# Kernel optimization log

Measured on AMD Instinct MI355X. Metric: run time of the kernel, lower is better.

## Reference

```python
import jax, jax.numpy as jnp
import numpy as np

# model dims
B, L, C, P, D, NB = 8, 512, 862, 96, 128, 2   # batch, seq_len, enc_in, pred_len, d_model, e_layers
I = 2 * D                                     # mLSTM inner (up-projection factor 2)
NH = 4                                        # mLSTM heads
DH = I // NH                                  # head dim
KDEC = 25                                     # series-decomp moving-average kernel
CK = 4                                        # causal conv kernel in mLSTM layer
EPS = 1e-5


def _ln(x, g):
    m = jnp.mean(x, -1, keepdims=True)
    v = jnp.var(x, -1, keepdims=True)
    return (x - m) * jax.lax.rsqrt(v + EPS) * g


def _mlstm_block(x, p):
    """Pre-LN residual mLSTM block (parallel stabilized formulation)."""
    (lng, Wup, bup, Wc, bc, Wq, Wk, Wv, Wi, bi, Wf, bf, mhg, skip, Wdn, bdn) = p
    Bn, S, _ = x.shape
    y = _ln(x, lng)
    up = y @ Wup + bup                       # [B,S,2I]
    x_in, z = jnp.split(up, 2, axis=-1)      # [B,S,I] each
    # causal depthwise conv (kernel CK) + SiLU
    xc = jax.lax.conv_general_dilated(
        x_in, Wc, window_strides=(1,), padding=((CK - 1, 0),),
        dimension_numbers=('NWC', 'WIO', 'NWC'), feature_group_count=I) + bc
    xc = jax.nn.silu(xc)
    q = xc @ Wq
    k = xc @ Wk
    v = x_in @ Wv
    g_in = jnp.concatenate([q, k, v], -1)    # [B,S,3I]
    ig = (g_in @ Wi + bi).transpose(0, 2, 1)  # [B,NH,S] input-gate preact
    fg = (g_in @ Wf + bf).transpose(0, 2, 1)  # [B,NH,S] forget-gate preact
    qh = q.reshape(Bn, S, NH, DH).transpose(0, 2, 1, 3)
    kh = k.reshape(Bn, S, NH, DH).transpose(0, 2, 1, 3) * (DH ** -0.5)
    vh = v.reshape(Bn, S, NH, DH).transpose(0, 2, 1, 3)
    logf = jax.nn.log_sigmoid(fg)            # [B,NH,S]
    cum = jnp.cumsum(logf, -1)               # inclusive cumsum
    # logD[t,s] = sum_{u=s+1..t} logf_u + i_s  (s<=t)
    logD = cum[..., :, None] - cum[..., None, :] + ig[..., None, :]
    mask = jnp.tril(jnp.ones((S, S), bool))
    logD = jnp.where(mask, logD, -jnp.inf)
    m = jnp.max(logD, -1, keepdims=True)     # row-wise stabilizer [B,NH,S,1]
    Dm = jnp.exp(logD - m)
    scores = jnp.einsum('bhtd,bhsd->bhts', qh, kh) * Dm
    norm = jnp.maximum(jnp.abs(jnp.sum(scores, -1, keepdims=True)), jnp.exp(-m))
    h = jnp.einsum('bhts,bhsd->bhtd', scores / norm, vh)  # [B,NH,S,DH]
    h = h.transpose(0, 2, 1, 3)              # [B,S,NH,DH]
    # multi-head layernorm (per-head, weight only)
    mu = jnp.mean(h, -1, keepdims=True)
    va = jnp.var(h, -1, keepdims=True)
    hn = ((h - mu) * jax.lax.rsqrt(va + EPS)).reshape(Bn, S, I) * mhg
    hs = (hn + skip * xc) * jax.nn.silu(z)
    return x + hs @ Wdn + bdn


def setup_inputs() -> dict:
    key = jax.random.key(0)
    ks = iter(jax.random.split(key, 32))
    f32 = jnp.float32
    def n(shape, s=0.02):
        return jax.random.normal(next(ks), shape, dtype=f32) * s
    inp = {
        'x_enc': jax.random.normal(next(ks), (B, L, C), f32),
        'x_mark_enc': jax.random.normal(next(ks), (B, L, 4), f32),
        'x_dec': jax.random.normal(next(ks), (B, P, C), f32),
        'x_mark_dec': jax.random.normal(next(ks), (B, P, 4), f32),
        # DLinear-style heads (init 1/seq_len as in the source)
        'Ws': jnp.full((P, L), 1.0 / L, dtype=f32), 'bs': jnp.zeros((P,), f32),
        'Wt': jnp.full((P, L), 1.0 / L, dtype=f32), 'bt': jnp.zeros((P,), f32),
        'Wp1': n((D, P)), 'bp1': jnp.zeros((D,), f32),
        'Wp2': n((P, D)), 'bp2': jnp.zeros((P,), f32),
        # stacked per-block mLSTM params
        'ln_g': jnp.ones((NB, D), f32),
        'Wup': n((NB, D, 2 * I)), 'bup': jnp.zeros((NB, 2 * I), f32),
        'Wconv': n((NB, CK, 1, I), 0.1), 'bconv': jnp.zeros((NB, I), f32),
        'Wq': n((NB, I, I)), 'Wk': n((NB, I, I)), 'Wv': n((NB, I, I)),
        'Wi': n((NB, 3 * I, NH)), 'bi': jnp.zeros((NB, NH), f32),
        'Wf': n((NB, 3 * I, NH)), 'bf': jnp.full((NB, NH), 3.0, dtype=f32),
        'mh_g': jnp.ones((NB, I), f32), 'skip': jnp.ones((NB, I), f32),
        'Wdn': n((NB, I, D)), 'bdn': jnp.zeros((NB, D), f32),
        'post_g': jnp.ones((D,), f32),
    }
    return inp


def reference(x_enc, x_mark_enc, x_dec, x_mark_dec, Ws, bs, Wt, bt, Wp1, bp1,
              Wp2, bp2, ln_g, Wup, bup, Wconv, bconv, Wq, Wk, Wv, Wi, bi, Wf,
              bf, mh_g, skip, Wdn, bdn, post_g):
    # series decomposition: edge-replicated moving average (kernel 25, stride 1)
    pad = (KDEC - 1) // 2
    front = jnp.repeat(x_enc[:, :1, :], pad, axis=1)
    end = jnp.repeat(x_enc[:, -1:, :], pad, axis=1)
    xp = jnp.concatenate([front, x_enc, end], axis=1)          # [B,L+24,C]
    cs = jnp.concatenate([jnp.zeros_like(xp[:, :1]), jnp.cumsum(xp, 1)], 1)
    mm = (cs[:, KDEC:, :] - cs[:, :-KDEC, :]) / KDEC           # [B,L,C]
    res = x_enc - mm
    si = res.transpose(0, 2, 1)                                # [B,C,L]
    ti = mm.transpose(0, 2, 1)
    x = (si @ Ws.T + bs) + (ti @ Wt.T + bt)                    # [B,C,P]
    x = x @ Wp1.T + bp1                                        # [B,C,D]
    for b in range(NB):
        x = _mlstm_block(x, (ln_g[b], Wup[b], bup[b], Wconv[b], bconv[b],
                             Wq[b], Wk[b], Wv[b], Wi[b], bi[b], Wf[b], bf[b],
                             mh_g[b], skip[b], Wdn[b], bdn[b]))
    x = _ln(x, post_g)
    x = x @ Wp2.T + bp2                                        # [B,C,P]
    return x.transpose(0, 2, 1)                                # [B,P,C]
```

## Files before the change

kernel.cpp:

```cpp
#include <hip/hip_runtime.h>
#include <math.h>

#define BB 8
#define LL 512
#define CC 862
#define PP 96
#define DD 128
#define II 256
#define NHH 4
#define DHH 64
#define SS 862
#define BC (BB*CC)
#define VTS 864
#define NITEMS2 896

typedef unsigned short u16;
using bf16x8 = __attribute__((ext_vector_type(8))) short;
using f32x4  = __attribute__((ext_vector_type(4))) float;

__device__ __forceinline__ u16 f2b(float x) {
  union { float f; unsigned u; } v; v.f = x;
  unsigned r = v.u + 0x7FFF + ((v.u >> 16) & 1);
  return (u16)(r >> 16);
}
__device__ __forceinline__ float b2f(u16 h) {
  union { unsigned u; float f; } v; v.u = ((unsigned)h) << 16;
  return v.f;
}

#define XCH(r, c) ((((c) ^ ((r) & 7)) << 3))

__global__ __launch_bounds__(256) void prep_kernel(
    const float* __restrict__ Wup, const float* __restrict__ Wq,
    const float* __restrict__ Wk, const float* __restrict__ Wv,
    const float* __restrict__ Wdn, const float* __restrict__ Ws,
    const float* __restrict__ Wt, const float* __restrict__ Wp1,
    const float* __restrict__ bs, const float* __restrict__ bt,
    const float* __restrict__ bp1, const float* __restrict__ Wi,
    const float* __restrict__ Wf,
    u16* __restrict__ WupT, u16* __restrict__ WqkT,
    u16* __restrict__ WvT, u16* __restrict__ WdnT,
    u16* __restrict__ BTh, float* __restrict__ hbias,
    float* __restrict__ Gc, float* __restrict__ Gv)
{
  int gb = blockIdx.x;
  int tid = threadIdx.x;
  if (gb < 640) {
    int bx = gb & 63, by = gb >> 6;
    const float* src; u16* dst; int R, Cn; float scl = 1.f;
    switch (by) {
      case 0: src = Wup;          dst = WupT;            R = 128; Cn = 512; break;
      case 1: src = Wup + 65536;  dst = WupT + 65536;    R = 128; Cn = 512; break;
      case 2: src = Wq;           dst = WqkT;            R = 256; Cn = 256; scl = 0.125f; break;
      case 3: src = Wk;           dst = WqkT + 65536;    R = 256; Cn = 256; break;
      case 4: src = Wq + 65536;   dst = WqkT + 131072;   R = 256; Cn = 256; scl = 0.125f; break;
      case 5: src = Wk + 65536;   dst = WqkT + 196608;   R = 256; Cn = 256; break;
      case 6: src = Wv;           dst = WvT;             R = 256; Cn = 256; break;
      case 7: src = Wv + 65536;   dst = WvT + 65536;     R = 256; Cn = 256; break;
      case 8: src = Wdn;          dst = WdnT;            R = 256; Cn = 128; break;
      default: src = Wdn + 32768; dst = WdnT + 32768;    R = 256; Cn = 128; break;
    }
    int tpr = Cn >> 5;
    int tx = bx % tpr, ty_ = bx / tpr;
    if (ty_ >= (R >> 5)) return;
    __shared__ float t[32][33];
    int r0 = ty_ * 32, c0 = tx * 32;
    int cr = tid >> 5, cc = tid & 31;
    #pragma unroll
    for (int rr = 0; rr < 4; ++rr)
      t[cr + rr * 8][cc] = src[(size_t)(r0 + cr + rr * 8) * Cn + c0 + cc];
    __syncthreads();
    #pragma unroll
    for (int rr = 0; rr < 4; ++rr)
      dst[(size_t)(c0 + cr + rr * 8) * R + r0 + cc] = f2b(t[cc][cr + rr * 8] * scl);
  } else if (gb < 1152) {
    int i2 = gb - 640;
    int d = i2 & 127, byy = i2 >> 7;
    int lp = byy * 256 + tid;
    const float* wp = Wp1 + d * 96;
    float acc = 0.f;
    if (lp < 512) {
      for (int p = 0; p < 96; ++p) acc += Ws[p * 512 + lp] * wp[p];
    } else {
      int l = lp - 512;
      for (int p = 0; p < 96; ++p) acc += (Wt[p * 512 + l] - Ws[p * 512 + l]) * wp[p];
    }
    BTh[(size_t)d * 1024 + lp] = f2b(acc);
  } else if (gb == 1152) {
    if (tid < 128) {
      float acc = bp1[tid];
      for (int p = 0; p < 96; ++p) acc += (bs[p] + bt[p]) * Wp1[tid * 96 + p];
      hbias[tid] = acc;
    }
  } else {
    int i2 = gb - 1153;
    int i = i2 & 255, blk = i2 >> 8;
    int j = tid;
    float wq = Wq[(size_t)blk * 65536 + i * 256 + j];
    float wk = Wk[(size_t)blk * 65536 + i * 256 + j];
    float wv = Wv[(size_t)blk * 65536 + i * 256 + j];
    const float* wi = Wi + blk * 3072;
    const float* wf = Wf + blk * 3072;
    float pc[8], pv[8];
    #pragma unroll
    for (int o = 0; o < 4; ++o) {
      pc[o]     = wq * wi[j * 4 + o] + wk * wi[(256 + j) * 4 + o];
      pc[4 + o] = wq * wf[j * 4 + o] + wk * wf[(256 + j) * 4 + o];
      pv[o]     = wv * wi[(512 + j) * 4 + o];
      pv[4 + o] = wv * wf[(512 + j) * 4 + o];
    }
    #pragma unroll
    for (int o = 0; o < 8; ++o)
      #pragma unroll
      for (int d = 1; d < 64; d <<= 1) {
        pc[o] += __shfl_xor(pc[o], d);
        pv[o] += __shfl_xor(pv[o], d);
      }
    __shared__ float red[4][16];
    int wv_ = j >> 6, lane = j & 63;
    if (lane == 0) {
      #pragma unroll
      for (int o = 0; o < 8; ++o) { red[wv_][o] = pc[o]; red[wv_][8 + o] = pv[o]; }
    }
    __syncthreads();
    if (j < 16) {
      float s4 = red[0][j] + red[1][j] + red[2][j] + red[3][j];
      if (j < 8) Gc[((size_t)blk * 256 + i) * 8 + j] = s4;
      else       Gv[((size_t)blk * 256 + i) * 8 + j - 8] = s4;
    }
  }
}

__global__ __launch_bounds__(256) void ta_kernel(
    const float* __restrict__ xe, u16* __restrict__ Ah)
{
  __shared__ float xel[16][545];
  __shared__ float mml[16][517];
  int tid = threadIdx.x;
  int b = blockIdx.x / 54, ct = blockIdx.x % 54;
  int c0 = ct * 16;
  for (int j = 0; j < 34; ++j) {
    int idx = tid + j * 256;
    if (idx < 8576) {
      int li = idx >> 4, cc = idx & 15;
      int l = li - 12; l = l < 0 ? 0 : (l > 511 ? 511 : l);
      int c = c0 + cc; if (c > 861) c = 861;
      xel[cc][li] = xe[((size_t)b * LL + l) * CC + c];
    }
  }
  __syncthreads();
  {
    int cl = tid & 15;
    int l0 = (tid >> 4) * 32;
    float win = 0.f;
    #pragma unroll 5
    for (int o = 0; o < 25; ++o) win += xel[cl][l0 + o];
    mml[cl][l0] = win * (1.f / 25.f);
    for (int i = 1; i < 32; ++i) {
      win += xel[cl][l0 + 24 + i] - xel[cl][l0 + i - 1];
      mml[cl][l0 + i] = win * (1.f / 25.f);
    }
  }
  __syncthreads();
  for (int j = 0; j < 32; ++j) {
    int idx = tid + j * 256;
    int cr = idx >> 9, l = idx & 511;
    int c = c0 + cr;
    if (c < CC) {
      size_t base = ((size_t)b * CC + c) * 1024;
      Ah[base + l] = f2b(xel[cr][12 + l]);
      Ah[base + 512 + l] = f2b(mml[cr][l]);
    }
  }
}

__device__ __forceinline__ void gemm_core(
    const u16* __restrict__ A, int lda, const u16* __restrict__ BT, int ldbt,
    int M, int K, int m0, int n0, int tid,
    u16 (*As0)[40], u16 (*As1)[40], u16 (*Bs0)[40], u16 (*Bs1)[40],
    f32x4 acc[2][2])
{
  int wv = tid >> 6, lane = tid & 63;
  int wr = wv >> 1, wc = wv & 1;
  int lrow = lane & 15, lk = lane >> 4;
  int arow = tid >> 2, aseg = tid & 3;
  for (int k0 = 0; k0 < K; k0 += 64) {
    int gm = m0 + arow; if (gm > M - 1) gm = M - 1;
    const u16* ap = &A[(size_t)gm * lda + k0 + aseg * 8];
    *(uint4*)&As0[arow][aseg * 8] = *(const uint4*)ap;
    *(uint4*)&As1[arow][aseg * 8] = *(const uint4*)(ap + 32);
    const u16* bp = &BT[(size_t)(n0 + arow) * ldbt + k0 + aseg * 8];
    *(uint4*)&Bs0[arow][aseg * 8] = *(const uint4*)bp;
    *(uint4*)&Bs1[arow][aseg * 8] = *(const uint4*)(bp + 32);
    __syncthreads();
    bf16x8 af[2], bfr[2];
    #pragma unroll
    for (int fm = 0; fm < 2; ++fm) af[fm] = *(const bf16x8*)&As0[wr * 32 + fm * 16 + lrow][lk * 8];
    #pragma unroll
    for (int fn = 0; fn < 2; ++fn) bfr[fn] = *(const bf16x8*)&Bs0[wc * 32 + fn * 16 + lrow][lk * 8];
    #pragma unroll
    for (int fm = 0; fm < 2; ++fm)
      #pragma unroll
      for (int fn = 0; fn < 2; ++fn)
        acc[fm][fn] = __builtin_amdgcn_mfma_f32_16x16x32_bf16(af[fm], bfr[fn], acc[fm][fn], 0, 0, 0);
    #pragma unroll
    for (int fm = 0; fm < 2; ++fm) af[fm] = *(const bf16x8*)&As1[wr * 32 + fm * 16 + lrow][lk * 8];
    #pragma unroll
    for (int fn = 0; fn < 2; ++fn) bfr[fn] = *(const bf16x8*)&Bs1[wc * 32 + fn * 16 + lrow][lk * 8];
    #pragma unroll
    for (int fm = 0; fm < 2; ++fm)
      #pragma unroll
      for (int fn = 0; fn < 2; ++fn)
        acc[fm][fn] = __builtin_amdgcn_mfma_f32_16x16x32_bf16(af[fm], bfr[fn], acc[fm][fn], 0, 0, 0);
    __syncthreads();
  }
}

template<int MODE>
__global__ __launch_bounds__(256) void gemm_bf16(
    const u16* __restrict__ A, int lda,
    const u16* __restrict__ BT, int ldbt,
    float* __restrict__ C, int ldc, const float* __restrict__ bias,
    int M, int N, int K)
{
  __shared__ u16 As0[64][40], As1[64][40];
  __shared__ u16 Bs0[64][40], Bs1[64][40];
  int tid = threadIdx.x;
  int m0 = blockIdx.y * 64, n0 = blockIdx.x * 64;
  f32x4 acc[2][2] = {};
  gemm_core(A, lda, BT, ldbt, M, K, m0, n0, tid, As0, As1, Bs0, Bs1, acc);
  int wv = tid >> 6, lane = tid & 63;
  int wr = wv >> 1, wc = wv & 1;
  int lrow = lane & 15, lk = lane >> 4;
  #pragma unroll
  for (int fm = 0; fm < 2; ++fm) {
    #pragma unroll
    for (int fn = 0; fn < 2; ++fn) {
      int col = n0 + wc * 32 + fn * 16 + lrow;
      #pragma unroll
      for (int r = 0; r < 4; ++r) {
        int row = m0 + wr * 32 + fm * 16 + lk * 4 + r;
        if (row < M) {
          float vv = acc[fm][fn][r];
          if (bias) vv += bias[col];
          float* cp = &C[(size_t)row * ldc + col];
          if (MODE == 1) vv += *cp;
          *cp = vv;
        }
      }
    }
  }
}

template<int MODE, int OUTF32, int FUSEC>
__global__ __launch_bounds__(256) void gemm_ln(
    const u16* __restrict__ A, int lda,
    const u16* __restrict__ BT, int ldbt,
    float* __restrict__ x, const float* __restrict__ bias,
    const float* __restrict__ g,
    float* __restrict__ y, u16* __restrict__ y_bf,
    int M, int K,
    const float* __restrict__ pacc, const float* __restrict__ pw,
    const float* __restrict__ cumf, const float* __restrict__ MMb,
    const float* __restrict__ up2, const float* __restrict__ xc2,
    const float* __restrict__ mhg, const float* __restrict__ skip)
{
  __shared__ u16 As0[32][40], As1[32][40];
  __shared__ u16 Bs0[128][40], Bs1[128][40];
  __shared__ float red_s[32][2], red_q[32][2];
  int tid = threadIdx.x;
  int m0 = blockIdx.x * 32;
  int wv = tid >> 6, lane = tid & 63;
  int wr = wv >> 1, wc = wv & 1;
  int lrow = lane & 15, lk = lane >> 4;
  f32x4 acc[4] = {};
  int arow = tid >> 3, aseg7 = tid & 7;
  int brow = tid >> 1, bhalf = tid & 1;
  for (int k0 = 0; k0 < K; k0 += 64) {
    int gm = m0 + arow; if (gm > M - 1) gm = M - 1;
    if (FUSEC == 0) {
      const u16* ap = &A[(size_t)gm * lda + k0];
      if (aseg7 < 4) *(uint4*)&As0[arow][aseg7 * 8] = *(const uint4*)(ap + aseg7 * 8);
      else           *(uint4*)&As1[arow][(aseg7 - 4) * 8] = *(const uint4*)(ap + 32 + (aseg7 - 4) * 8);
    } else {
      int bb = gm / SS, sx = gm - bb * SS;
      int hh = k0 >> 6;
      size_t bhS = ((size_t)bb * NHH + hh) * SS + sx;
      float wsum = pw[bhS] + pw[(size_t)BB * NHH * SS + bhS];
      float nfl = __expf(-(cumf[bhS] + MMb[bhS]));
      float rden = 1.f / fmaxf(fabsf(wsum), nfl);
      int colb = k0 + aseg7 * 8;
      const float* p0 = &pacc[(size_t)gm * II + colb];
      const float* p1 = p0 + (size_t)BC * II;
      float hv[8], sr = 0.f, sq2 = 0.f;
      #pragma unroll
      for (int j = 0; j < 8; ++j) {
        hv[j] = (p0[j] + p1[j]) * rden;
        sr += hv[j]; sq2 += hv[j] * hv[j];
      }
      sr += __shfl_xor(sr, 1); sq2 += __shfl_xor(sq2, 1);
      sr += __shfl_xor(sr, 2); sq2 += __shfl_xor(sq2, 2);
      sr += __shfl_xor(sr, 4); sq2 += __shfl_xor(sq2, 4);
      float mu = sr * (1.f / 64.f);
      float var = sq2 * (1.f / 64.f) - mu * mu;
      float rr2 = rsqrtf(var + 1e-5f);
      u16 o8[8];
      #pragma unroll
      for (int j = 0; j < 8; ++j) {
        int col = colb + j;
        float hn = (hv[j] - mu) * rr2 * mhg[col];
        float z = up2[(size_t)gm * 512 + 256 + col];
        float sil = z / (1.f + __expf(-z));
        o8[j] = f2b((hn + skip[col] * xc2[(size_t)gm * II + col]) * sil);
      }
      if (aseg7 < 4) *(uint4*)&As0[arow][aseg7 * 8] = *(const uint4*)o8;
      else           *(uint4*)&As1[arow][(aseg7 - 4) * 8] = *(const uint4*)o8;
    }
    const u16* bp = &BT[(size_t)brow * ldbt + k0];
    #pragma unroll
    for (int j = 0; j < 2; ++j) {
      int seg = bhalf * 2 + j;
      *(uint4*)&Bs0[brow][seg * 8] = *(const uint4*)(bp + seg * 8);
      *(uint4*)&Bs1[brow][seg * 8] = *(const uint4*)(bp + 32 + seg * 8);
    }
    __syncthreads();
    bf16x8 af, bfr[4];
    af = *(const bf16x8*)&As0[wr * 16 + lrow][lk * 8];
    #pragma unroll
    for (int fn = 0; fn < 4; ++fn) bfr[fn] = *(const bf16x8*)&Bs0[wc * 64 + fn * 16 + lrow][lk * 8];
    #pragma unroll
    for (int fn = 0; fn < 4; ++fn)
      acc[fn] = __builtin_amdgcn_mfma_f32_16x16x32_bf16(af, bfr[fn], acc[fn], 0, 0, 0);
    af = *(const bf16x8*)&As1[wr * 16 + lrow][lk * 8];
    #pragma unroll
    for (int fn = 0; fn < 4; ++fn) bfr[fn] = *(const bf16x8*)&Bs1[wc * 64 + fn * 16 + lrow][lk * 8];
    #pragma unroll
    for (int fn = 0; fn < 4; ++fn)
      acc[fn] = __builtin_amdgcn_mfma_f32_16x16x32_bf16(af, bfr[fn], acc[fn], 0, 0, 0);
    __syncthreads();
  }
  #pragma unroll
  for (int r = 0; r < 4; ++r) {
    int lrid = wr * 16 + lk * 4 + r;
    int grow = m0 + lrid;
    float sr = 0.f, sq = 0.f;
    #pragma unroll
    for (int fn = 0; fn < 4; ++fn) {
      int col = wc * 64 + fn * 16 + lrow;
      float vv = acc[fn][r] + bias[col];
      if (MODE == 1) vv += x[(size_t)grow * DD + col];
      acc[fn][r] = vv;
      if (grow < M) x[(size_t)grow * DD + col] = vv;
      sr += vv; sq += vv * vv;
    }
    sr += __shfl_xor(sr, 1); sq += __shfl_xor(sq, 1);
    sr += __shfl_xor(sr, 2); sq += __shfl_xor(sq, 2);
    sr += __shfl_xor(sr, 4); sq += __shfl_xor(sq, 4);
    sr += __shfl_xor(sr, 8); sq += __shfl_xor(sq, 8);
    if (lrow == 0) { red_s[lrid][wc] = sr; red_q[lrid][wc] = sq; }
  }
  __syncthreads();
  #pragma unroll
  for (int r = 0; r < 4; ++r) {
    int lrid = wr * 16 + lk * 4 + r;
    int grow = m0 + lrid;
    if (grow >= M) continue;
    float s = red_s[lrid][0] + red_s[lrid][1];
    float q = red_q[lrid][0] + red_q[lrid][1];
    float mean = s * (1.f / 128.f);
    float var = q * (1.f / 128.f) - mean * mean;
    float rr = rsqrtf(var + 1e-5f);
    #pragma unroll
    for (int fn = 0; fn < 4; ++fn) {
      int col = wc * 64 + fn * 16 + lrow;
      float out = (acc[fn][r] - mean) * rr * g[col];
      if (OUTF32) y[(size_t)grow * DD + col] = out;
      else        y_bf[(size_t)grow * DD + col] = f2b(out);
    }
  }
}

__device__ __forceinline__ float logsig(float x) {
  return fminf(x, 0.f) - log1pf(__expf(-fabsf(x)));
}

__global__ __launch_bounds__(256) void qkv_scan_kernel(
    const u16* __restrict__ xc_bf, const u16* __restrict__ xin_bf,
    const u16* __restrict__ WqkT, const u16* __restrict__ WvT,
    u16* __restrict__ qkh, u16* __restrict__ qkl,
    u16* __restrict__ vhT, u16* __restrict__ vlT,
    const float* __restrict__ fg, const float* __restrict__ ig,
    float* __restrict__ cumf, float* __restrict__ aa, float* __restrict__ MMb)
{
  __shared__ u16 As0[64][40], As1[64][40];
  __shared__ u16 Bs0[64][40], Bs1[64][40];
  int tid = threadIdx.x;
  int bx = blockIdx.x;
  if (bx >= 1296) {
    if (tid >= 64) return;
    int bh = bx - 1296;
    int lane = tid;
    const float* f = fg + (size_t)bh * SS;
    const float* gg = ig + (size_t)bh * SS;
    int s0 = lane * 14, s1 = s0 + 14; if (s1 > SS) s1 = SS;
    float loc = 0.f;
    for (int s = s0; s < s1; ++s) loc += logsig(f[s]);
    float v = loc;
    #pragma unroll
    for (int d = 1; d < 64; d <<= 1) { float o = __shfl_up(v, d); if (lane >= d) v += o; }
    float run = v - loc;
    float lmax = -1e30f;
    for (int s = s0; s < s1; ++s) {
      run += logsig(f[s]);
      cumf[(size_t)bh * SS + s] = run;
      float a = gg[s] - run;
      aa[(size_t)bh * SS + s] = a;
      lmax = fmaxf(lmax, a);
    }
    float mv = lmax;
    #pragma unroll
    for (int d = 1; d < 64; d <<= 1) { float o = __shfl_up(mv, d); if (lane >= d) mv = fmaxf(mv, o); }
    float em = __shfl_up(mv, 1);
    if (lane == 0) em = -1e30f;
    float runm = em;
    for (int s = s0; s < s1; ++s) {
      runm = fmaxf(runm, aa[(size_t)bh * SS + s]);
      MMb[(size_t)bh * SS + s] = runm;
    }
    return;
  }
  int m0 = (bx / 12) * 64;
  int nrole = bx % 12;
  bool is_qk = nrole < 8;
  int n0 = (is_qk ? nrole : nrole - 8) * 64;
  const u16* A  = is_qk ? xc_bf : xin_bf;
  const u16* BT = is_qk ? WqkT : WvT;
  f32x4 acc[2][2] = {};
  gemm_core(A, 256, BT, 256, BC, 256, m0, n0, tid, As0, As1, Bs0, Bs1, acc);
  int wv = tid >> 6, lane = tid & 63;
  int wr = wv >> 1, wc = wv & 1;
  int lrow = lane & 15, lk = lane >> 4;
  #pragma unroll
  for (int fm = 0; fm < 2; ++fm) {
    #pragma unroll
    for (int fn = 0; fn < 2; ++fn) {
      int col = n0 + wc * 32 + fn * 16 + lrow;
      int rbase = m0 + wr * 32 + fm * 16 + lk * 4;
      if (is_qk) {
        #pragma unroll
        for (int r = 0; r < 4; ++r) {
          int row = rbase + r;
          if (row < BC) {
            float vv = acc[fm][fn][r];
            u16 hi = f2b(vv);
            u16 lo = f2b(vv - b2f(hi));
            qkh[(size_t)row * 512 + col] = hi;
            qkl[(size_t)row * 512 + col] = lo;
          }
        }
      } else {
        u16 hi4[4], lo4[4];
        #pragma unroll
        for (int r = 0; r < 4; ++r) {
          float vv = acc[fm][fn][r];
          hi4[r] = f2b(vv);
          lo4[r] = f2b(vv - b2f(hi4[r]));
        }
        int bb0 = rbase / SS, s0_ = rbase - bb0 * SS;
        int bb3 = (rbase + 3) / SS;
        if (bb0 == bb3 && rbase + 3 < BC) {
          size_t o = ((size_t)bb0 * II + col) * VTS + s0_;
          *(unsigned*)&vhT[o]     = (unsigned)hi4[0] | ((unsigned)hi4[1] << 16);
          *(unsigned*)&vhT[o + 2] = (unsigned)hi4[2] | ((unsigned)hi4[3] << 16);
          *(unsigned*)&vlT[o]     = (unsigned)lo4[0] | ((unsigned)lo4[1] << 16);
          *(unsigned*)&vlT[o + 2] = (unsigned)lo4[2] | ((unsigned)lo4[3] << 16);
        } else {
          #pragma unroll
          for (int r = 0; r < 4; ++r) {
            int row = rbase + r;
            if (row < BC) {
              int bb = row / SS, s = row - bb * SS;
              size_t o = ((size_t)bb * II + col) * VTS + s;
              vhT[o] = hi4[r];
              vlT[o] = lo4[r];
            }
          }
        }
      }
    }
  }
}

__global__ __launch_bounds__(256) void conv_gates_kernel(
    const float* __restrict__ up, const float* __restrict__ Wc,
    const float* __restrict__ bc, const float* __restrict__ Gc,
    const float* __restrict__ Gv, const float* __restrict__ bi,
    const float* __restrict__ bfp,
    float* __restrict__ xc, u16* __restrict__ xc_bf, u16* __restrict__ xin_bf,
    float* __restrict__ ig, float* __restrict__ fg)
{
  __shared__ float red[4][8];
  int row = blockIdx.x;
  int i = threadIdx.x;
  int b = row / SS, s = row - b * SS;
  float acc = bc[i];
  float xin = 0.f;
  #pragma unroll
  for (int w2 = 0; w2 < 4; ++w2) {
    int sp = s - 3 + w2;
    if (sp >= 0) {
      float uv = up[((size_t)b * SS + sp) * 512 + i];
      acc += uv * Wc[w2 * 256 + i];
      if (w2 == 3) xin = uv;
    }
  }
  float sg = 1.f / (1.f + __expf(-acc));
  float val = acc * sg;
  xc[(size_t)row * II + i] = val;
  xc_bf[(size_t)row * II + i] = f2b(val);
  xin_bf[(size_t)row * II + i] = f2b(xin);
  float p[8];
  const float* gci = &Gc[i * 8];
  const float* gvi = &Gv[i * 8];
  #pragma unroll
  for (int o = 0; o < 8; ++o) p[o] = val * gci[o] + xin * gvi[o];
  #pragma unroll
  for (int o = 0; o < 8; ++o)
    #pragma unroll
    for (int d = 1; d < 64; d <<= 1) p[o] += __shfl_xor(p[o], d);
  int wv = i >> 6, lane = i & 63;
  if (lane == 0) {
    #pragma unroll
    for (int o = 0; o < 8; ++o) red[wv][o] = p[o];
  }
  __syncthreads();
  if (i < 8) {
    float sum = red[0][i] + red[1][i] + red[2][i] + red[3][i];
    if (i < 4) ig[((size_t)b * NHH + i) * SS + s] = sum + bi[i];
    else       fg[((size_t)b * NHH + i - 4) * SS + s] = sum + bfp[i - 4];
  }
}

__global__ __launch_bounds__(256) void attn_kernel(
    const u16* __restrict__ qkh, const u16* __restrict__ qkl,
    const u16* __restrict__ vhT, const u16* __restrict__ vlT,
    const float* __restrict__ aab, const float* __restrict__ MMb,
    float* __restrict__ pacc, float* __restrict__ pw)
{
  __shared__ u16 KWh[64][64], KWl[64][64];
  __shared__ u16 Vh[64][64], Vl[64][64];
  __shared__ float a_lds[64];
  int tid = threadIdx.x;
  int wv = tid >> 6, lane = tid & 63;
  int lr = lane & 15, lg = lane >> 4;
  int item = blockIdx.x;
  int pp = item >> 5;
  int tb = 13 - (pp >> 1);
  int part = pp & 1;
  int h = item & 3, b = (item >> 2) & 7;
  int t0 = tb * 64;
  int nt = tb + 1;
  int nt0 = (nt + 1) >> 1;
  int st_begin = part ? nt0 : 0;
  int st_end   = part ? nt : nt0;
  const float* aabh = aab + ((size_t)b * NHH + h) * SS;
  const float* Mbh  = MMb + ((size_t)b * NHH + h) * SS;

  int tq = t0 + wv * 16 + lr; if (tq > SS - 1) tq = SS - 1;
  const u16* qrow_h = qkh + ((size_t)b * SS + tq) * 512 + h * 64;
  const u16* qrow_l = qkl + ((size_t)b * SS + tq) * 512 + h * 64;
  bf16x8 qh0 = *(const bf16x8*)(qrow_h + lg * 8);
  bf16x8 qh1 = *(const bf16x8*)(qrow_h + 32 + lg * 8);
  bf16x8 ql0 = *(const bf16x8*)(qrow_l + lg * 8);
  bf16x8 ql1 = *(const bf16x8*)(qrow_l + 32 + lg * 8);

  float Mt[4];
  #pragma unroll
  for (int r = 0; r < 4; ++r) {
    int t = t0 + wv * 16 + lg * 4 + r; int tc = t < SS ? t : SS - 1;
    Mt[r] = Mbh[tc];
  }

  int row = tid >> 2, seg = tid & 3;
  const u16* vrow_h = vhT + ((size_t)(b * II + h * 64 + row)) * VTS + seg * 16;
  const u16* vrow_l = vlT + ((size_t)(b * II + h * 64 + row)) * VTS + seg * 16;

  f32x4 hacc[4] = {};
  float wsum[4] = {0.f, 0.f, 0.f, 0.f};

  uint4 rk0, rk1, rk2, rk3, rv0, rv1, rv2, rv3;
  float ra = -1e30f;
  if (st_begin < st_end) {
    int sg = st_begin * 64 + row;
    int sc = sg < SS ? sg : SS - 1;
    const u16* kp  = qkh + ((size_t)b * SS + sc) * 512 + 256 + h * 64 + seg * 16;
    const u16* klp = qkl + ((size_t)b * SS + sc) * 512 + 256 + h * 64 + seg * 16;
    rk0 = *(const uint4*)kp;  rk1 = *(const uint4*)(kp + 8);
    rk2 = *(const uint4*)klp; rk3 = *(const uint4*)(klp + 8);
    int sn = st_begin * 64;
    rv0 = *(const uint4*)(vrow_h + sn); rv1 = *(const uint4*)(vrow_h + sn + 8);
    rv2 = *(const uint4*)(vrow_l + sn); rv3 = *(const uint4*)(vrow_l + sn + 8);
    if (tid < 64) ra = (sn + tid < SS) ? aabh[sn + tid] : -1e30f;
  }

  for (int st = st_begin; st < st_end; ++st) {
    int s0 = st * 64;
    __syncthreads();
    *(uint4*)&KWh[row][XCH(row, 2 * seg)]     = rk0;
    *(uint4*)&KWh[row][XCH(row, 2 * seg + 1)] = rk1;
    *(uint4*)&KWl[row][XCH(row, 2 * seg)]     = rk2;
    *(uint4*)&KWl[row][XCH(row, 2 * seg + 1)] = rk3;
    *(uint4*)&Vh[row][XCH(row, 2 * seg)]     = rv0;
    *(uint4*)&Vh[row][XCH(row, 2 * seg + 1)] = rv1;
    *(uint4*)&Vl[row][XCH(row, 2 * seg)]     = rv2;
    *(uint4*)&Vl[row][XCH(row, 2 * seg + 1)] = rv3;
    if (tid < 64) a_lds[tid] = ra;
    if (st + 1 < st_end) {
      int sn = s0 + 64;
      int sg = sn + row;
      int sc = sg < SS ? sg : SS - 1;
      const u16* kp  = qkh + ((size_t)b * SS + sc) * 512 + 256 + h * 64 + seg * 16;
      const u16* klp = qkl + ((size_t)b * SS + sc) * 512 + 256 + h * 64 + seg * 16;
      rk0 = *(const uint4*)kp;  rk1 = *(const uint4*)(kp + 8);
      rk2 = *(const uint4*)klp; rk3 = *(const uint4*)(klp + 8);
      rv0 = *(const uint4*)(vrow_h + sn); rv1 = *(const uint4*)(vrow_h + sn + 8);
      rv2 = *(const uint4*)(vrow_l + sn); rv3 = *(const uint4*)(vrow_l + sn + 8);
      if (tid < 64) ra = (sn + tid < SS) ? aabh[sn + tid] : -1e30f;
    }
    __syncthreads();
    float am = a_lds[lane];
    #pragma unroll
    for (int dd = 1; dd < 64; dd <<= 1) am = fmaxf(am, __shfl_xor(am, dd));
    f32x4 p[4];
    #pragma unroll
    for (int sf = 0; sf < 4; ++sf) {
      int sr = sf * 16 + lr;
      bf16x8 kh0 = *(const bf16x8*)&KWh[sr][XCH(sr, lg)];
      bf16x8 kh1 = *(const bf16x8*)&KWh[sr][XCH(sr, lg + 4)];
      bf16x8 kl0 = *(const bf16x8*)&KWl[sr][XCH(sr, lg)];
      bf16x8 kl1 = *(const bf16x8*)&KWl[sr][XCH(sr, lg + 4)];
      f32x4 acc = {};
      acc = __builtin_amdgcn_mfma_f32_16x16x32_bf16(qh0, kl0, acc, 0, 0, 0);
      acc = __builtin_amdgcn_mfma_f32_16x16x32_bf16(qh1, kl1, acc, 0, 0, 0);
      acc = __builtin_amdgcn_mfma_f32_16x16x32_bf16(ql0, kh0, acc, 0, 0, 0);
      acc = __builtin_amdgcn_mfma_f32_16x16x32_bf16(ql1, kh1, acc, 0, 0, 0);
      acc = __builtin_amdgcn_mfma_f32_16x16x32_bf16(qh0, kh0, acc, 0, 0, 0);
      acc = __builtin_amdgcn_mfma_f32_16x16x32_bf16(qh1, kh1, acc, 0, 0, 0);
      p[sf] = acc;
    }
    __syncthreads();
    float ee[4], ft[4];
    #pragma unroll
    for (int sf = 0; sf < 4; ++sf) ee[sf] = __expf(a_lds[sf * 16 + lr] - am);
    #pragma unroll
    for (int r = 0; r < 4; ++r) ft[r] = __expf(fminf(am - Mt[r], 80.f));
    #pragma unroll
    for (int sf = 0; sf < 4; ++sf) {
      int s = s0 + sf * 16 + lr;
      int sc_ = sf * 2 + (lr >> 3), sb = lr & 7;
      #pragma unroll
      for (int r = 0; r < 4; ++r) {
        int tl_ = wv * 16 + lg * 4 + r;
        int t = t0 + tl_;
        float wval = (s <= t) ? p[sf][r] * ee[sf] * ft[r] : 0.f;
        wsum[r] += wval;
        u16 hi_ = f2b(wval);
        u16 lo_ = f2b(wval - b2f(hi_));
        KWh[tl_][XCH(tl_, sc_) + sb] = hi_;
        KWl[tl_][XCH(tl_, sc_) + sb] = lo_;
      }
    }
    __syncthreads();
    int tr = wv * 16 + lr;
    bf16x8 wh0 = *(const bf16x8*)&KWh[tr][XCH(tr, lg)];
    bf16x8 wh1 = *(const bf16x8*)&KWh[tr][XCH(tr, lg + 4)];
    bf16x8 wl0 = *(const bf16x8*)&KWl[tr][XCH(tr, lg)];
    bf16x8 wl1 = *(const bf16x8*)&KWl[tr][XCH(tr, lg + 4)];
    #pragma unroll
    for (int df = 0; df < 4; ++df) {
      int dr = df * 16 + lr;
      bf16x8 vh0 = *(const bf16x8*)&Vh[dr][XCH(dr, lg)];
      bf16x8 vh1 = *(const bf16x8*)&Vh[dr][XCH(dr, lg + 4)];
      bf16x8 vl0 = *(const bf16x8*)&Vl[dr][XCH(dr, lg)];
      bf16x8 vl1 = *(const bf16x8*)&Vl[dr][XCH(dr, lg + 4)];
      f32x4 a2 = hacc[df];
      a2 = __builtin_amdgcn_mfma_f32_16x16x32_bf16(wh0, vl0, a2, 0, 0, 0);
      a2 = __builtin_amdgcn_mfma_f32_16x16x32_bf16(wh1, vl1, a2, 0, 0, 0);
      a2 = __builtin_amdgcn_mfma_f32_16x16x32_bf16(wl0, vh0, a2, 0, 0, 0);
      a2 = __builtin_amdgcn_mfma_f32_16x16x32_bf16(wl1, vh1, a2, 0, 0, 0);
      a2 = __builtin_amdgcn_mfma_f32_16x16x32_bf16(wh0, vh0, a2, 0, 0, 0);
      a2 = __builtin_amdgcn_mfma_f32_16x16x32_bf16(wh1, vh1, a2, 0, 0, 0);
      hacc[df] = a2;
    }
  }
  #pragma unroll
  for (int r = 0; r < 4; ++r) {
    float sgn = wsum[r];
    sgn += __shfl_xor(sgn, 1); sgn += __shfl_xor(sgn, 2);
    sgn += __shfl_xor(sgn, 4); sgn += __shfl_xor(sgn, 8);
    wsum[r] = sgn;
  }
  float* pa = pacc + (size_t)part * BC * II;
  #pragma unroll
  for (int r = 0; r < 4; ++r) {
    int t = t0 + wv * 16 + lg * 4 + r;
    if (t < SS) {
      #pragma unroll
      for (int df = 0; df < 4; ++df)
        pa[((size_t)b * SS + t) * II + h * 64 + df * 16 + lr] = hacc[df][r];
      if (lr == 0)
        pw[(((size_t)part * BB + b) * NHH + h) * SS + t] = wsum[r];
    }
  }
}

__global__ __launch_bounds__(256) void final_kernel(
    const float* __restrict__ y, const float* __restrict__ Wp2,
    const float* __restrict__ bp2, float* __restrict__ out)
{
  __shared__ float yl[32 * 132];
  __shared__ float ol[96 * 32];
  int tid = threadIdx.x;
  int blk = blockIdx.x;
  int b = blk / 27, ct = blk % 27;
  int c0 = ct * 32;
  int nc = CC - c0; if (nc > 32) nc = 32;
  for (int j = 0; j < 16; ++j) {
    int idx = tid + j * 256;
    int cl = idx >> 7, d2 = idx & 127;
    yl[cl * 132 + d2] = (cl < nc) ? y[((size_t)b * CC + c0 + cl) * DD + d2] : 0.f;
  }
  __syncthreads();
  for (int j = 0; j < 12; ++j) {
    int o = tid + j * 256;
    int p = o >> 5, cl = o & 31;
    const float* wr = Wp2 + p * 128;
    float acc = bp2[p];
    #pragma unroll 8
    for (int d0 = 0; d0 < 128; d0 += 4) {
      float4 yv = *(const float4*)&yl[cl * 132 + d0];
      float4 wv = *(const float4*)&wr[d0];
      acc += yv.x * wv.x + yv.y * wv.y + yv.z * wv.z + yv.w * wv.w;
    }
    ol[p * 32 + cl] = acc;
  }
  __syncthreads();
  for (int j = 0; j < 12; ++j) {
    int o = tid + j * 256;
    int p = o >> 5, cl = o & 31;
    if (cl < nc) out[(size_t)b * PP * CC + (size_t)p * CC + c0 + cl] = ol[p * 32 + cl];
  }
}

extern "C" void kernel_launch(void* const* d_in, const int* in_sizes, int n_in,
                              void* d_out, int out_size, void* d_ws, size_t ws_size,
                              hipStream_t stream) {
  const float* xe   = (const float*)d_in[0];
  const float* Ws   = (const float*)d_in[4];
  const float* bs   = (const float*)d_in[5];
  const float* Wt_  = (const float*)d_in[6];
  const float* bt   = (const float*)d_in[7];
  const float* Wp1  = (const float*)d_in[8];
  const float* bp1  = (const float*)d_in[9];
  const float* Wp2  = (const float*)d_in[10];
  const float* bp2  = (const float*)d_in[11];
  const float* lng  = (const float*)d_in[12];
  const float* Wup  = (const float*)d_in[13];
  const float* bup  = (const float*)d_in[14];
  const float* Wcv  = (const float*)d_in[15];
  const float* bcv  = (const float*)d_in[16];
  const float* Wq   = (const float*)d_in[17];
  const float* Wk   = (const float*)d_in[18];
  const float* Wv   = (const float*)d_in[19];
  const float* Wi   = (const float*)d_in[20];
  const float* bi   = (const float*)d_in[21];
  const float* Wf   = (const float*)d_in[22];
  const float* bf_  = (const float*)d_in[23];
  const float* mhg  = (const float*)d_in[24];
  const float* skp  = (const float*)d_in[25];
  const float* Wdn  = (const float*)d_in[26];
  const float* bdn  = (const float*)d_in[27];
  const float* pg   = (const float*)d_in[28];
  float* out = (float*)d_out;

  float* w   = (float*)d_ws;
  float* x   = w;
  float* y   = x   + 882688;
  float* up  = y   + 882688;
  float* xc  = up  + 3530752;
  float* pacc = xc + 1765376;
  float* pw  = pacc + 3530752;
  float* ig  = pw  + 55168;
  float* fg  = ig  + 27584;
  float* cum = fg  + 27584;
  float* aab = cum + 27584;
  float* MMb = aab + 27584;
  float* hbias = MMb + 27584;
  float* Gc  = hbias + 128;
  float* Gv  = Gc + 4096;
  u16* ub    = (u16*)(Gv + 4096);
  u16* y_bf  = ub;            ub += 6896 * 128;
  u16* xc_bf = ub;            ub += 6896 * 256;
  u16* xin_bf = ub;           ub += 6896 * 256;
  u16* qkh   = ub;            ub += 6896 * 512;
  u16* qkl   = ub;            ub += 6896 * 512;
  u16* vhT   = ub;            ub += 8 * 256 * VTS;
  u16* vlT   = ub;            ub += 8 * 256 * VTS;
  u16* BTh   = ub;            ub += 131072;
  u16* WupT  = ub;            ub += 131072;
  u16* WqkT  = ub;            ub += 262144;
  u16* WvT   = ub;            ub += 131072;
  u16* WdnT  = ub;            ub += 65536;
  u16* Ah = (u16*)up;

  prep_kernel<<<1665, 256, 0, stream>>>(
      Wup, Wq, Wk, Wv, Wdn, Ws, Wt_, Wp1, bs, bt, bp1, Wi, Wf,
      WupT, WqkT, WvT, WdnT, BTh, hbias, Gc, Gv);

  ta_kernel<<<432, 256, 0, stream>>>(xe, Ah);
  gemm_ln<0, 0, 0><<<216, 256, 0, stream>>>(
      Ah, 1024, BTh, 1024, x, hbias, lng, nullptr, y_bf, BC, 1024,
      nullptr, nullptr, nullptr, nullptr, nullptr, nullptr, nullptr, nullptr);

  for (int blk = 0; blk < 2; ++blk) {
    gemm_bf16<0><<<dim3(8, 108), 256, 0, stream>>>(
        y_bf, 128, WupT + blk * 65536, 128, up, 512, bup + blk * 512, BC, 512, 128);
    conv_gates_kernel<<<6896, 256, 0, stream>>>(
        up, Wcv + blk * 1024, bcv + blk * 256, Gc + blk * 2048, Gv + blk * 2048,
        bi + blk * 4, bf_ + blk * 4, xc, xc_bf, xin_bf, ig, fg);
    qkv_scan_kernel<<<1328, 256, 0, stream>>>(
        xc_bf, xin_bf, WqkT + blk * 131072, WvT + blk * 65536,
        qkh, qkl, vhT, vlT, fg, ig, cum, aab, MMb);
    attn_kernel<<<NITEMS2, 256, 0, stream>>>(qkh, qkl, vhT, vlT, aab, MMb, pacc, pw);
    if (blk == 0)
      gemm_ln<1, 0, 1><<<216, 256, 0, stream>>>(
          nullptr, 0, WdnT, 256, x, bdn, lng + 128, nullptr, y_bf, BC, 256,
          pacc, pw, cum, MMb, up, xc, mhg, skp);
    else
      gemm_ln<1, 1, 1><<<216, 256, 0, stream>>>(
          nullptr, 0, WdnT + 32768, 256, x, bdn + 128, pg, y, nullptr, BC, 256,
          pacc, pw, cum, MMb, up, xc, mhg + 256, skp + 256);
  }

  final_kernel<<<216, 256, 0, stream>>>(y, Wp2, bp2, out);
}
```

Measured before the change: 255.3 us.

## Fuse decomposition into prep kernel and output projection into final LN GEMM

The series-decomposition kernel is merged into the weight-prep kernel as extra blocks, so both run in one launch. The final kernel is also removed: the last LayerNorm GEMM writes its normalized rows to shared memory and computes the Wp2 projection directly into the output. This removes two kernel launches and the fp32 round trip of the final activations through global memory. In exchange, larger shared-memory allocations apply to all blocks of the merged kernels, which may reduce occupancy.

```diff
diff --git a/kernel.cpp b/kernel.cpp
--- a/kernel.cpp
+++ b/kernel.cpp
@@ -30,22 +30,66 @@
 
 #define XCH(r, c) ((((c) ^ ((r) & 7)) << 3))
 
-__global__ __launch_bounds__(256) void prep_kernel(
+__global__ __launch_bounds__(256) void prep_ta_kernel(
     const float* __restrict__ Wup, const float* __restrict__ Wq,
     const float* __restrict__ Wk, const float* __restrict__ Wv,
     const float* __restrict__ Wdn, const float* __restrict__ Ws,
     const float* __restrict__ Wt, const float* __restrict__ Wp1,
     const float* __restrict__ bs, const float* __restrict__ bt,
     const float* __restrict__ bp1, const float* __restrict__ Wi,
-    const float* __restrict__ Wf,
+    const float* __restrict__ Wf, const float* __restrict__ xe,
     u16* __restrict__ WupT, u16* __restrict__ WqkT,
     u16* __restrict__ WvT, u16* __restrict__ WdnT,
     u16* __restrict__ BTh, float* __restrict__ hbias,
-    float* __restrict__ Gc, float* __restrict__ Gv)
+    float* __restrict__ Gc, float* __restrict__ Gv,
+    u16* __restrict__ Ah)
 {
+  __shared__ float smem[16 * 545 + 16 * 517];
   int gb = blockIdx.x;
   int tid = threadIdx.x;
+  if (gb >= 1665) {
+    float (*xel)[545] = (float(*)[545])smem;
+    float (*mml)[517] = (float(*)[517])(smem + 16 * 545);
+    int bx = gb - 1665;
+    int b = bx / 54, ct = bx % 54;
+    int c0 = ct * 16;
+    for (int j = 0; j < 34; ++j) {
+      int idx = tid + j * 256;
+      if (idx < 8576) {
+        int li = idx >> 4, cc = idx & 15;
+        int l = li - 12; l = l < 0 ? 0 : (l > 511 ? 511 : l);
+        int c = c0 + cc; if (c > 861) c = 861;
+        xel[cc][li] = xe[((size_t)b * LL + l) * CC + c];
+      }
+    }
+    __syncthreads();
+    {
+      int cl = tid & 15;
+      int l0 = (tid >> 4) * 32;
+      float win = 0.f;
+      #pragma unroll 5
+      for (int o = 0; o < 25; ++o) win += xel[cl][l0 + o];
+      mml[cl][l0] = win * (1.f / 25.f);
+      for (int i = 1; i < 32; ++i) {
+        win += xel[cl][l0 + 24 + i] - xel[cl][l0 + i - 1];
+        mml[cl][l0 + i] = win * (1.f / 25.f);
+      }
+    }
+    __syncthreads();
+    for (int j = 0; j < 32; ++j) {
+      int idx = tid + j * 256;
+      int cr = idx >> 9, l = idx & 511;
+      int c = c0 + cr;
+      if (c < CC) {
+        size_t base = ((size_t)b * CC + c) * 1024;
+        Ah[base + l] = f2b(xel[cr][12 + l]);
+        Ah[base + 512 + l] = f2b(mml[cr][l]);
+      }
+    }
+    return;
+  }
   if (gb < 640) {
+    float (*t)[33] = (float(*)[33])smem;
     int bx = gb & 63, by = gb >> 6;
     const float* src; u16* dst; int R, Cn; float scl = 1.f;
     switch (by) {
@@ -63,7 +107,6 @@
     int tpr = Cn >> 5;
     int tx = bx % tpr, ty_ = bx / tpr;
     if (ty_ >= (R >> 5)) return;
-    __shared__ float t[32][33];
     int r0 = ty_ * 32, c0 = tx * 32;
     int cr = tid >> 5, cc = tid & 31;
     #pragma unroll
@@ -93,6 +136,7 @@
       hbias[tid] = acc;
     }
   } else {
+    float (*red)[16] = (float(*)[16])smem;
     int i2 = gb - 1153;
     int i = i2 & 255, blk = i2 >> 8;
     int j = tid;
@@ -116,7 +160,6 @@
         pc[o] += __shfl_xor(pc[o], d);
         pv[o] += __shfl_xor(pv[o], d);
       }
-    __shared__ float red[4][16];
     int wv_ = j >> 6, lane = j & 63;
     if (lane == 0) {
       #pragma unroll
@@ -127,49 +170,6 @@
       float s4 = red[0][j] + red[1][j] + red[2][j] + red[3][j];
       if (j < 8) Gc[((size_t)blk * 256 + i) * 8 + j] = s4;
       else       Gv[((size_t)blk * 256 + i) * 8 + j - 8] = s4;
-    }
-  }
-}
-
-__global__ __launch_bounds__(256) void ta_kernel(
-    const float* __restrict__ xe, u16* __restrict__ Ah)
-{
-  __shared__ float xel[16][545];
-  __shared__ float mml[16][517];
-  int tid = threadIdx.x;
-  int b = blockIdx.x / 54, ct = blockIdx.x % 54;
-  int c0 = ct * 16;
-  for (int j = 0; j < 34; ++j) {
-    int idx = tid + j * 256;
-    if (idx < 8576) {
-      int li = idx >> 4, cc = idx & 15;
-      int l = li - 12; l = l < 0 ? 0 : (l > 511 ? 511 : l);
-      int c = c0 + cc; if (c > 861) c = 861;
-      xel[cc][li] = xe[((size_t)b * LL + l) * CC + c];
-    }
-  }
-  __syncthreads();
-  {
-    int cl = tid & 15;
-    int l0 = (tid >> 4) * 32;
-    float win = 0.f;
-    #pragma unroll 5
-    for (int o = 0; o < 25; ++o) win += xel[cl][l0 + o];
-    mml[cl][l0] = win * (1.f / 25.f);
-    for (int i = 1; i < 32; ++i) {
-      win += xel[cl][l0 + 24 + i] - xel[cl][l0 + i - 1];
-      mml[cl][l0 + i] = win * (1.f / 25.f);
-    }
-  }
-  __syncthreads();
-  for (int j = 0; j < 32; ++j) {
-    int idx = tid + j * 256;
-    int cr = idx >> 9, l = idx & 511;
-    int c = c0 + cr;
-    if (c < CC) {
-      size_t base = ((size_t)b * CC + c) * 1024;
-      Ah[base + l] = f2b(xel[cr][12 + l]);
-      Ah[base + 512 + l] = f2b(mml[cr][l]);
     }
   }
 }
@@ -252,7 +252,7 @@
   }
 }
 
-template<int MODE, int OUTF32, int FUSEC>
+template<int MODE, int OUTF32, int FUSEC, int FINAL>
 __global__ __launch_bounds__(256) void gemm_ln(
     const u16* __restrict__ A, int lda,
     const u16* __restrict__ BT, int ldbt,
@@ -263,11 +263,14 @@
     const float* __restrict__ pacc, const float* __restrict__ pw,
     const float* __restrict__ cumf, const float* __restrict__ MMb,
     const float* __restrict__ up2, const float* __restrict__ xc2,
-    const float* __restrict__ mhg, const float* __restrict__ skip)
+    const float* __restrict__ mhg, const float* __restrict__ skip,
+    const float* __restrict__ Wp2, const float* __restrict__ bp2,
+    float* __restrict__ out)
 {
   __shared__ u16 As0[32][40], As1[32][40];
   __shared__ u16 Bs0[128][40], Bs1[128][40];
   __shared__ float red_s[32][2], red_q[32][2];
+  __shared__ float yl[32][132];
   int tid = threadIdx.x;
   int m0 = blockIdx.x * 32;
   int wv = tid >> 6, lane = tid & 63;
@@ -364,7 +367,7 @@
   for (int r = 0; r < 4; ++r) {
     int lrid = wr * 16 + lk * 4 + r;
     int grow = m0 + lrid;
-    if (grow >= M) continue;
+    if (FINAL == 0 && grow >= M) continue;
     float s = red_s[lrid][0] + red_s[lrid][1];
     float q = red_q[lrid][0] + red_q[lrid][1];
     float mean = s * (1.f / 128.f);
@@ -373,9 +376,33 @@
     #pragma unroll
     for (int fn = 0; fn < 4; ++fn) {
       int col = wc * 64 + fn * 16 + lrow;
-      float out = (acc[fn][r] - mean) * rr * g[col];
-      if (OUTF32) y[(size_t)grow * DD + col] = out;
-      else        y_bf[(size_t)grow * DD + col] = f2b(out);
+      float outv = (acc[fn][r] - mean) * rr * g[col];
+      if (FINAL) {
+        yl[lrid][col] = outv;
+      } else if (OUTF32) {
+        y[(size_t)grow * DD + col] = outv;
+      } else {
+        y_bf[(size_t)grow * DD + col] = f2b(outv);
+      }
+    }
+  }
+  if (FINAL) {
+    __syncthreads();
+    for (int j = 0; j < 12; ++j) {
+      int o = tid + j * 256;
+      int p = o >> 5, cl = o & 31;
+      int grow = m0 + cl;
+      if (grow >= M) continue;
+      const float* wr2 = Wp2 + p * 128;
+      float accf = bp2[p];
+      #pragma unroll 8
+      for (int d0 = 0; d0 < 128; d0 += 4) {
+        float4 yv = *(const float4*)&yl[cl][d0];
+        float4 wv2 = *(const float4*)&wr2[d0];
+        accf += yv.x * wv2.x + yv.y * wv2.y + yv.z * wv2.z + yv.w * wv2.w;
+      }
+      int b = grow / SS, c = grow - b * SS;
+      out[(size_t)b * PP * CC + (size_t)p * CC + c] = accf;
     }
   }
 }
@@ -714,44 +741,6 @@
   }
 }
 
-__global__ __launch_bounds__(256) void final_kernel(
-    const float* __restrict__ y, const float* __restrict__ Wp2,
-    const float* __restrict__ bp2, float* __restrict__ out)
-{
-  __shared__ float yl[32 * 132];
-  __shared__ float ol[96 * 32];
-  int tid = threadIdx.x;
-  int blk = blockIdx.x;
-  int b = blk / 27, ct = blk % 27;
-  int c0 = ct * 32;
-  int nc = CC - c0; if (nc > 32) nc = 32;
-  for (int j = 0; j < 16; ++j) {
-    int idx = tid + j * 256;
-    int cl = idx >> 7, d2 = idx & 127;
-    yl[cl * 132 + d2] = (cl < nc) ? y[((size_t)b * CC + c0 + cl) * DD + d2] : 0.f;
-  }
-  __syncthreads();
-  for (int j = 0; j < 12; ++j) {
-    int o = tid + j * 256;
-    int p = o >> 5, cl = o & 31;
-    const float* wr = Wp2 + p * 128;
-    float acc = bp2[p];
-    #pragma unroll 8
-    for (int d0 = 0; d0 < 128; d0 += 4) {
-      float4 yv = *(const float4*)&yl[cl * 132 + d0];
-      float4 wv = *(const float4*)&wr[d0];
-      acc += yv.x * wv.x + yv.y * wv.y + yv.z * wv.z + yv.w * wv.w;
-    }
-    ol[p * 32 + cl] = acc;
-  }
-  __syncthreads();
-  for (int j = 0; j < 12; ++j) {
-    int o = tid + j * 256;
-    int p = o >> 5, cl = o & 31;
-    if (cl < nc) out[(size_t)b * PP * CC + (size_t)p * CC + c0 + cl] = ol[p * 32 + cl];
-  }
-}
-
 extern "C" void kernel_launch(void* const* d_in, const int* in_sizes, int n_in,
                               void* d_out, int out_size, void* d_ws, size_t ws_size,
                               hipStream_t stream) {
@@ -813,14 +802,14 @@
   u16* WdnT  = ub;            ub += 65536;
   u16* Ah = (u16*)up;
 
-  prep_kernel<<<1665, 256, 0, stream>>>(
-      Wup, Wq, Wk, Wv, Wdn, Ws, Wt_, Wp1, bs, bt, bp1, Wi, Wf,
-      WupT, WqkT, WvT, WdnT, BTh, hbias, Gc, Gv);
-
-  ta_kernel<<<432, 256, 0, stream>>>(xe, Ah);
-  gemm_ln<0, 0, 0><<<216, 256, 0, stream>>>(
+  prep_ta_kernel<<<2097, 256, 0, stream>>>(
+      Wup, Wq, Wk, Wv, Wdn, Ws, Wt_, Wp1, bs, bt, bp1, Wi, Wf, xe,
+      WupT, WqkT, WvT, WdnT, BTh, hbias, Gc, Gv, Ah);
+
+  gemm_ln<0, 0, 0, 0><<<216, 256, 0, stream>>>(
       Ah, 1024, BTh, 1024, x, hbias, lng, nullptr, y_bf, BC, 1024,
-      nullptr, nullptr, nullptr, nullptr, nullptr, nullptr, nullptr, nullptr);
+      nullptr, nullptr, nullptr, nullptr, nullptr, nullptr, nullptr, nullptr,
+      nullptr, nullptr, nullptr);
 
   for (int blk = 0; blk < 2; ++blk) {
     gemm_bf16<0><<<dim3(8, 108), 256, 0, stream>>>(
@@ -833,14 +822,12 @@
         qkh, qkl, vhT, vlT, fg, ig, cum, aab, MMb);
     attn_kernel<<<NITEMS2, 256, 0, stream>>>(qkh, qkl, vhT, vlT, aab, MMb, pacc, pw);
     if (blk == 0)
-      gemm_ln<1, 0, 1><<<216, 256, 0, stream>>>(
+      gemm_ln<1, 0, 1, 0><<<216, 256, 0, stream>>>(
           nullptr, 0, WdnT, 256, x, bdn, lng + 128, nullptr, y_bf, BC, 256,
-          pacc, pw, cum, MMb, up, xc, mhg, skp);
+          pacc, pw, cum, MMb, up, xc, mhg, skp, nullptr, nullptr, nullptr);
     else
-      gemm_ln<1, 1, 1><<<216, 256, 0, stream>>>(
-          nullptr, 0, WdnT + 32768, 256, x, bdn + 128, pg, y, nullptr, BC, 256,
-          pacc, pw, cum, MMb, up, xc, mhg + 256, skp + 256);
-  }
-
-  final_kernel<<<216, 256, 0, stream>>>(y, Wp2, bp2, out);
-}
+      gemm_ln<1, 0, 1, 1><<<216, 256, 0, stream>>>(
+          nullptr, 0, WdnT + 32768, 256, x, bdn + 128, pg, nullptr, nullptr, BC, 256,
+          pacc, pw, cum, MMb, up, xc, mhg + 256, skp + 256, Wp2, bp2, out);
+  }
+}
```

After: 250.5 us. No clear change (-1.9%).
